# Performance work log

Measured on AMD Instinct MI355X. Metric: run time of the kernel, lower is better.

The kernel has to match this reference:

```python
import jax, jax.numpy as jnp
import numpy as np

DT = 0.1
GRAVITY = 9.81
DENSITY = 1028.0
ZVEC = jnp.array([0.0, 0.0, 1.0], dtype=jnp.float32)


def _skew(v):
    # v: [k,3] -> [k,3,3] skew-symmetric matrix (matches A/B/C column construction)
    x, y, z = v[..., 0], v[..., 1], v[..., 2]
    o = jnp.zeros_like(x)
    r0 = jnp.stack([o, -z, y], -1)
    r1 = jnp.stack([z, o, -x], -1)
    r2 = jnp.stack([-y, x, o], -1)
    return jnp.stack([r0, r1, r2], -2)


def _body2inertial(pose):
    # pose: [k,7]; quat stored as (x,y,z,w) in pose[:,3:7]
    q = pose[:, 3:7]
    x, y, z, w = q[:, 0], q[:, 1], q[:, 2], q[:, 3]
    r0 = jnp.stack([1 - 2 * (y * y + z * z), 2 * (x * y - z * w), 2 * (x * z + y * w)], -1)
    r1 = jnp.stack([2 * (x * y + z * w), 1 - 2 * (x * x + z * z), 2 * (y * z - x * w)], -1)
    r2 = jnp.stack([2 * (x * z - y * w), 2 * (y * z + x * w), 1 - 2 * (x * x + y * y)], -1)
    rot = jnp.stack([r0, r1, r2], -2)  # [k,3,3]
    t = 0.5 * jnp.stack([
        jnp.stack([-x, -y, -z], -1),
        jnp.stack([w, -z, y], -1),
        jnp.stack([z, w, -x], -1),
        jnp.stack([-y, x, w], -1)], -2)  # [k,4,3]
    return rot, t


def _restoring(rot, mass, volume, cog, cob):
    fng = -mass * GRAVITY * ZVEC              # (3,)
    fnb = volume * DENSITY * GRAVITY * ZVEC   # (3,)
    # rotItoB = rot^T -> rot^T @ f == einsum('kji,j->ki')
    fbg = jnp.einsum('kji,j->ki', rot, fng)
    fbb = jnp.einsum('kji,j->ki', rot, fnb)
    mbg = jnp.cross(cog, fbg)
    mbb = jnp.cross(cob, fbb)
    return -jnp.concatenate([fbg + fbb, mbg + mbb], -1)  # [k,6]


def _damping(v, linDamp, linDampFow, quadDamp):
    eye6 = jnp.eye(6, dtype=v.dtype)
    D = -linDamp - v[:, :, None] * linDampFow
    return D - quadDamp * (jnp.abs(v)[:, :, None] * eye6)  # [k,6,6]


def _coriolis(v, mTot):
    M = mTot[0]
    mv_top = jnp.einsum('ij,kj->ki', M[0:3, 0:3], v[:, 0:3]) + jnp.einsum('ij,kj->ki', M[0:3, 3:6], v[:, 3:6])
    mv_bot = jnp.einsum('ij,kj->ki', M[3:6, 0:3], v[:, 0:3]) + jnp.einsum('ij,kj->ki', M[3:6, 3:6], v[:, 3:6])
    s12 = -_skew(mv_top)
    s22 = -_skew(mv_bot)
    z33 = jnp.zeros_like(s12)
    r1 = jnp.concatenate([z33, s12], -1)
    r2 = jnp.concatenate([s12, s22], -1)  # note: source uses s12 (not s12^T) in lower-left, reproduced faithfully
    return jnp.concatenate([r1, r2], -2)  # [k,6,6]


def _dot(x, u, mass, volume, cog, cob, mTot, linDamp, linDampFow, quadDamp):
    p, v = x[:, 0:7], x[:, 7:13]
    rot, t = _body2inertial(p)
    # jacobian is block-diag [[rot,0],[0,t]] -> apply blocks directly
    pDot_lin = jnp.einsum('kij,kj->ki', rot, v[:, 0:3])  # [k,3]
    pDot_ang = jnp.einsum('kij,kj->ki', t, v[:, 3:6])    # [k,4]
    D = _damping(v, linDamp, linDampFow, quadDamp)
    C = _coriolis(v, mTot)
    Dv = jnp.einsum('kij,kj->ki', D, v)
    Cv = jnp.einsum('kij,kj->ki', C, v)
    g = _restoring(rot, mass, volume, cog, cob)
    rhs = u - Cv - Dv - g                      # [k,6]
    vDot = jnp.linalg.solve(mTot[0], rhs.T).T  # single shared 6x6 solve
    return jnp.concatenate([pDot_lin, pDot_ang, vDot], -1)  # [k,13]


def _norm_quat(xs):
    q = xs[:, 3:7]
    q = q / jnp.linalg.norm(q, axis=-1, keepdims=True)
    return xs.at[:, 3:7].set(q)


def reference(x, u, mass, volume, cog, cob, mTot, linDamp, linDampFow, quadDamp):
    # RK2 integration step (rk=2 default)
    k1 = _dot(x, u, mass, volume, cog, cob, mTot, linDamp, linDampFow, quadDamp)
    k2 = _dot(x + k1 * DT, u, mass, volume, cog, cob, mTot, linDamp, linDampFow, quadDamp)
    return _norm_quat(x + (DT / 2.0) * (k1 + k2))


def setup_inputs() -> dict:
    key = jax.random.key(0)
    kx, ku = jax.random.split(key)
    K = 524288
    x = jax.random.normal(kx, (K, 13), dtype=jnp.float32)
    u = jax.random.normal(ku, (K, 6), dtype=jnp.float32)
    mass = jnp.array([100.0], dtype=jnp.float32)
    volume = jnp.array([1.0], dtype=jnp.float32)
    cog = jnp.zeros((1, 3), dtype=jnp.float32)
    cob = jnp.array([[0.0, 0.0, 0.2]], dtype=jnp.float32)
    rb = np.zeros((6, 6), dtype=np.float32)
    rb[0:3, 0:3] = 100.0 * np.eye(3, dtype=np.float32)
    ma = 100.0 * np.eye(6, dtype=np.float32) + 1e-7      # default Ma (+1e-7 on every entry)
    mTot = jnp.asarray(rb + ma)[None]                    # [1,6,6]
    linDamp = jnp.diag(jnp.array([-70.0, -70.0, -700.0, -300.0, -300.0, -100.0], dtype=jnp.float32))[None]
    linDampFow = jnp.zeros((1, 6, 6), dtype=jnp.float32)
    quadDamp = jnp.diag(jnp.array([-740.0, -990.0, -1800.0, -670.0, -770.0, -520.0], dtype=jnp.float32))[None]
    return {"x": x, "u": u, "mass": mass, "volume": volume, "cog": cog, "cob": cob,
            "mTot": mTot, "linDamp": linDamp, "linDampFow": linDampFow, "quadDamp": quadDamp}
```

## Files before the change

kernel.cpp:

```cpp
#include <hip/hip_runtime.h>
#include <math.h>


__device__ __forceinline__ float fast_rcp(float x) {
    float r = __builtin_amdgcn_rcpf(x);
    return r * (2.0f - x * r);
}

__device__ __forceinline__ void fossen_dot(const float* __restrict__ X,
                                           const float* __restrict__ U,
                                           const float* __restrict__ smi,
                                           const float* __restrict__ mTot,
                                           const float* __restrict__ linDamp,
                                           const float* __restrict__ linDampFow,
                                           const float* __restrict__ qdiag,
                                           const float* __restrict__ cgcb,
                                           float fgz, float fbz,
                                           float* __restrict__ xd)
{
    const float qx = X[3], qy = X[4], qz = X[5], qw = X[6];
    const float r00 = 1.f - 2.f*(qy*qy + qz*qz);
    const float r01 = 2.f*(qx*qy - qz*qw);
    const float r02 = 2.f*(qx*qz + qy*qw);
    const float r10 = 2.f*(qx*qy + qz*qw);
    const float r11 = 1.f - 2.f*(qx*qx + qz*qz);
    const float r12 = 2.f*(qy*qz - qx*qw);
    const float r20 = 2.f*(qx*qz - qy*qw);
    const float r21 = 2.f*(qy*qz + qx*qw);
    const float r22 = 1.f - 2.f*(qx*qx + qy*qy);

    const float v0 = X[7],  v1 = X[8],  v2 = X[9];
    const float v3 = X[10], v4 = X[11], v5 = X[12];

    xd[0] = r00*v0 + r01*v1 + r02*v2;
    xd[1] = r10*v0 + r11*v1 + r12*v2;
    xd[2] = r20*v0 + r21*v1 + r22*v2;
    xd[3] = 0.5f*(-qx*v3 - qy*v4 - qz*v5);
    xd[4] = 0.5f*( qw*v3 - qz*v4 + qy*v5);
    xd[5] = 0.5f*( qz*v3 + qw*v4 - qx*v5);
    xd[6] = 0.5f*(-qy*v3 + qx*v4 + qw*v5);

    const float v[6] = {v0, v1, v2, v3, v4, v5};

    float P[6];
#pragma unroll
    for (int i = 0; i < 6; ++i) {
        float ld = 0.f, ldf = 0.f;
#pragma unroll
        for (int j = 0; j < 6; ++j) {
            ld  += linDamp[i*6 + j]    * v[j];
            ldf += linDampFow[i*6 + j] * v[j];
        }
        P[i] = ld + v[i]*ldf + qdiag[i] * fabsf(v[i]) * v[i];
    }

    float mv[6];
#pragma unroll
    for (int i = 0; i < 6; ++i) {
        float s = 0.f;
#pragma unroll
        for (int j = 0; j < 6; ++j) s += mTot[i*6 + j] * v[j];
        mv[i] = s;
    }
    float Cv[6];
    Cv[0] = -(mv[1]*v5 - mv[2]*v4);
    Cv[1] = -(mv[2]*v3 - mv[0]*v5);
    Cv[2] = -(mv[0]*v4 - mv[1]*v3);
    Cv[3] = -(mv[1]*v2 - mv[2]*v1) - (mv[4]*v5 - mv[5]*v4);
    Cv[4] = -(mv[2]*v0 - mv[0]*v2) - (mv[5]*v3 - mv[3]*v5);
    Cv[5] = -(mv[0]*v1 - mv[1]*v0) - (mv[3]*v4 - mv[4]*v3);

    const float fb0 = r20*fgz, fb1 = r21*fgz, fb2 = r22*fgz;
    const float bb0 = r20*fbz, bb1 = r21*fbz, bb2 = r22*fbz;
    const float cgx = cgcb[0], cgy = cgcb[1], cgz = cgcb[2];
    const float cbx = cgcb[3], cby = cgcb[4], cbz = cgcb[5];
    const float m0 = cgy*fb2 - cgz*fb1 + cby*bb2 - cbz*bb1;
    const float m1 = cgz*fb0 - cgx*fb2 + cbz*bb0 - cbx*bb2;
    const float m2 = cgx*fb1 - cgy*fb0 + cbx*bb1 - cby*bb0;
    const float g[6] = { -(fb0+bb0), -(fb1+bb1), -(fb2+bb2), -m0, -m1, -m2 };

    float rhs[6];
#pragma unroll
    for (int i = 0; i < 6; ++i) rhs[i] = U[i] - Cv[i] + P[i] - g[i];

#pragma unroll
    for (int i = 0; i < 6; ++i) {
        float s = 0.f;
#pragma unroll
        for (int j = 0; j < 6; ++j) s += smi[i*6 + j] * rhs[j];
        xd[7+i] = s;
    }
}

__global__ void __launch_bounds__(256, 4)
auv_rk2_fused(const float* __restrict__ x, const float* __restrict__ u,
              const float* __restrict__ mass, const float* __restrict__ volume,
              const float* __restrict__ cog, const float* __restrict__ cob,
              const float* __restrict__ mTot, const float* __restrict__ linDamp,
              const float* __restrict__ linDampFow,
              const float* __restrict__ quadDamp,
              float* __restrict__ out, int K)
{
    __shared__ float sx[256 * 13];
    __shared__ float smi[36];
    const int tid   = threadIdx.x;
    const int base  = blockIdx.x * 256;
    const int nElem = min(256, K - base);

    if (nElem == 256) {
        const float* gx = x + (size_t)base * 13;
#pragma unroll
        for (int it = 0; it < 3; ++it) {
            const int k = it*256 + tid;
            __builtin_amdgcn_global_load_lds(
                (const __attribute__((address_space(1))) void*)(gx + (size_t)k*4),
                (__attribute__((address_space(3))) void*)(&sx[k*4]), 16, 0, 0);
        }
        if (tid < 64) {
            const int k = 768 + tid;
            __builtin_amdgcn_global_load_lds(
                (const __attribute__((address_space(1))) void*)(gx + (size_t)k*4),
                (__attribute__((address_space(3))) void*)(&sx[k*4]), 16, 0, 0);
        }
    } else {
        for (int k = tid; k < nElem*13; k += 256) sx[k] = x[(size_t)base*13 + k];
    }

    float U[6];
    if (tid < nElem) {
        const float* gu = u + (size_t)(base + tid) * 6;
        const float2 a2 = *(const float2*)(gu);
        const float2 b2 = *(const float2*)(gu + 2);
        const float2 c2 = *(const float2*)(gu + 4);
        U[0]=a2.x; U[1]=a2.y; U[2]=b2.x; U[3]=b2.y; U[4]=c2.x; U[5]=c2.y;
    }

    float qdiag[6], cgcb[6];
#pragma unroll
    for (int i = 0; i < 6; ++i) qdiag[i] = quadDamp[i*6 + i];
#pragma unroll
    for (int i = 0; i < 3; ++i) { cgcb[i] = cog[i]; cgcb[3+i] = cob[i]; }
    const float fgz = -mass[0] * 9.81f;
    const float fbz =  volume[0] * 1028.0f * 9.81f;

    if (tid == 0) {
        float a[36], Mi[36];
#pragma unroll
        for (int i = 0; i < 36; ++i) a[i] = mTot[i];
#pragma unroll
        for (int i = 0; i < 36; ++i) Mi[i] = 0.f;
#pragma unroll
        for (int i = 0; i < 6; ++i) Mi[i*6 + i] = 1.f;
#pragma unroll
        for (int col = 0; col < 6; ++col) {
            const float d = fast_rcp(a[col*6 + col]);
#pragma unroll
            for (int j = 0; j < 6; ++j) { a[col*6+j] *= d; Mi[col*6+j] *= d; }
#pragma unroll
            for (int r = 0; r < 6; ++r) {
                if (r == col) continue;
                const float f = a[r*6 + col];
#pragma unroll
                for (int j = 0; j < 6; ++j) {
                    a[r*6+j]  -= f * a[col*6+j];
                    Mi[r*6+j] -= f * Mi[col*6+j];
                }
            }
        }
#pragma unroll
        for (int i = 0; i < 36; ++i) smi[i] = Mi[i];
    }

    __syncthreads();

    if (tid < nElem) {
        float X[13];
#pragma unroll
        for (int j = 0; j < 13; ++j) X[j] = sx[tid*13 + j];

        float k1[13], X2[13], k2[13], Y[13];
        fossen_dot(X, U, smi, mTot, linDamp, linDampFow, qdiag, cgcb, fgz, fbz, k1);
#pragma unroll
        for (int j = 0; j < 13; ++j) X2[j] = X[j] + 0.1f * k1[j];
        fossen_dot(X2, U, smi, mTot, linDamp, linDampFow, qdiag, cgcb, fgz, fbz, k2);
#pragma unroll
        for (int j = 0; j < 13; ++j) Y[j] = X[j] + 0.05f * (k1[j] + k2[j]);

        const float nq  = Y[3]*Y[3] + Y[4]*Y[4] + Y[5]*Y[5] + Y[6]*Y[6];
        float inv = __builtin_amdgcn_rsqf(nq);
        inv = inv * (1.5f - 0.5f * nq * inv * inv);
        Y[3] *= inv; Y[4] *= inv; Y[5] *= inv; Y[6] *= inv;

#pragma unroll
        for (int j = 0; j < 13; ++j) sx[tid*13 + j] = Y[j];
    }
    __syncthreads();

    if (nElem == 256) {
        float4*       go = (float4*)(out + (size_t)base * 13);
        const float4* s4 = (const float4*)sx;
#pragma unroll
        for (int it = 0; it < 3; ++it) go[it*256 + tid] = s4[it*256 + tid];
        if (tid < 64) go[768 + tid] = s4[768 + tid];
    } else {
        for (int k = tid; k < nElem*13; k += 256) out[(size_t)base*13 + k] = sx[k];
    }
}

extern "C" void kernel_launch(void* const* d_in, const int* in_sizes, int n_in,
                              void* d_out, int out_size, void* d_ws, size_t ws_size,
                              hipStream_t stream)
{
    const float* x          = (const float*)d_in[0];
    const float* u          = (const float*)d_in[1];
    const float* mass       = (const float*)d_in[2];
    const float* volume     = (const float*)d_in[3];
    const float* cog        = (const float*)d_in[4];
    const float* cob        = (const float*)d_in[5];
    const float* mTot       = (const float*)d_in[6];
    const float* linDamp    = (const float*)d_in[7];
    const float* linDampFow = (const float*)d_in[8];
    const float* quadDamp   = (const float*)d_in[9];
    float*       out        = (float*)d_out;

    const int K = in_sizes[0] / 13;
    const int blocks = (K + 255) / 256;
    auv_rk2_fused<<<blocks, 256, 0, stream>>>(x, u, mass, volume, cog, cob,
                                              mTot, linDamp, linDampFow,
                                              quadDamp, out, K);
}
```

Before: 115.6 us.

## Add sparsity fast paths for damping and per-wave output stores

Detects at runtime whether linDamp is diagonal and linDampFow is all zero, and skips the full 6x6 products when they are. Each wavefront now stages and writes back its own 64 rows, so the block-wide barrier before the output store is replaced by a wave-local LDS waitcnt. The inverse mass matrix is padded to stride 8 so each row loads as a float4 plus a float2, and launch bounds are raised to 8 blocks per CU. The general matrix path is kept as a fallback. The per-thread scan of 72 global matrix entries is new overhead, and the added code may raise register pressure against the higher occupancy target.

```diff
diff --git a/kernel.cpp b/kernel.cpp
--- a/kernel.cpp
+++ b/kernel.cpp
@@ -14,8 +14,10 @@
                                            const float* __restrict__ linDamp,
                                            const float* __restrict__ linDampFow,
                                            const float* __restrict__ qdiag,
+                                           const float* __restrict__ lddiag,
                                            const float* __restrict__ cgcb,
                                            float fgz, float fbz,
+                                           bool ldDiag, bool ldfZero,
                                            float* __restrict__ xd)
 {
     const float qx = X[3], qy = X[4], qz = X[5], qw = X[6];
@@ -44,14 +46,26 @@
 
     float P[6];
 #pragma unroll
-    for (int i = 0; i < 6; ++i) {
-        float ld = 0.f, ldf = 0.f;
-#pragma unroll
-        for (int j = 0; j < 6; ++j) {
-            ld  += linDamp[i*6 + j]    * v[j];
-            ldf += linDampFow[i*6 + j] * v[j];
-        }
-        P[i] = ld + v[i]*ldf + qdiag[i] * fabsf(v[i]) * v[i];
+    for (int i = 0; i < 6; ++i)
+        P[i] = lddiag[i]*v[i] + qdiag[i]*fabsf(v[i])*v[i];
+    if (!ldDiag) {
+#pragma unroll
+        for (int i = 0; i < 6; ++i) {
+            float ld = 0.f;
+#pragma unroll
+            for (int j = 0; j < 6; ++j)
+                if (j != i) ld += linDamp[i*6 + j] * v[j];
+            P[i] += ld;
+        }
+    }
+    if (!ldfZero) {
+#pragma unroll
+        for (int i = 0; i < 6; ++i) {
+            float ldf = 0.f;
+#pragma unroll
+            for (int j = 0; j < 6; ++j) ldf += linDampFow[i*6 + j] * v[j];
+            P[i] += v[i]*ldf;
+        }
     }
 
     float mv[6];
@@ -85,14 +99,14 @@
 
 #pragma unroll
     for (int i = 0; i < 6; ++i) {
-        float s = 0.f;
-#pragma unroll
-        for (int j = 0; j < 6; ++j) s += smi[i*6 + j] * rhs[j];
-        xd[7+i] = s;
-    }
-}
-
-__global__ void __launch_bounds__(256, 4)
+        const float4 m4 = *(const float4*)(&smi[i*8]);
+        const float2 m2 = *(const float2*)(&smi[i*8 + 4]);
+        xd[7+i] = m4.x*rhs[0] + m4.y*rhs[1] + m4.z*rhs[2] + m4.w*rhs[3]
+                + m2.x*rhs[4] + m2.y*rhs[5];
+    }
+}
+
+__global__ void __launch_bounds__(256, 8)
 auv_rk2_fused(const float* __restrict__ x, const float* __restrict__ u,
               const float* __restrict__ mass, const float* __restrict__ volume,
               const float* __restrict__ cog, const float* __restrict__ cob,
@@ -102,8 +116,11 @@
               float* __restrict__ out, int K)
 {
     __shared__ float sx[256 * 13];
-    __shared__ float smi[36];
+    __shared__ float smi[48];
     const int tid   = threadIdx.x;
+    const int w     = tid >> 6;
+    const int l     = tid & 63;
+    const int wbase = w * 208;
     const int base  = blockIdx.x * 256;
     const int nElem = min(256, K - base);
 
@@ -111,13 +128,13 @@
         const float* gx = x + (size_t)base * 13;
 #pragma unroll
         for (int it = 0; it < 3; ++it) {
-            const int k = it*256 + tid;
+            const int k = wbase + it*64 + l;
             __builtin_amdgcn_global_load_lds(
                 (const __attribute__((address_space(1))) void*)(gx + (size_t)k*4),
                 (__attribute__((address_space(3))) void*)(&sx[k*4]), 16, 0, 0);
         }
-        if (tid < 64) {
-            const int k = 768 + tid;
+        if (l < 16) {
+            const int k = wbase + 192 + l;
             __builtin_amdgcn_global_load_lds(
                 (const __attribute__((address_space(1))) void*)(gx + (size_t)k*4),
                 (__attribute__((address_space(3))) void*)(&sx[k*4]), 16, 0, 0);
@@ -135,13 +152,22 @@
         U[0]=a2.x; U[1]=a2.y; U[2]=b2.x; U[3]=b2.y; U[4]=c2.x; U[5]=c2.y;
     }
 
-    float qdiag[6], cgcb[6];
-#pragma unroll
-    for (int i = 0; i < 6; ++i) qdiag[i] = quadDamp[i*6 + i];
+    float qdiag[6], lddiag[6], cgcb[6];
+#pragma unroll
+    for (int i = 0; i < 6; ++i) { qdiag[i] = quadDamp[i*6+i]; lddiag[i] = linDamp[i*6+i]; }
 #pragma unroll
     for (int i = 0; i < 3; ++i) { cgcb[i] = cog[i]; cgcb[3+i] = cob[i]; }
     const float fgz = -mass[0] * 9.81f;
     const float fbz =  volume[0] * 1028.0f * 9.81f;
+
+    bool ldDiag = true, ldfZero = true;
+#pragma unroll
+    for (int i = 0; i < 6; ++i)
+#pragma unroll
+        for (int j = 0; j < 6; ++j) {
+            ldfZero = ldfZero && (linDampFow[i*6+j] == 0.0f);
+            if (i != j) ldDiag = ldDiag && (linDamp[i*6+j] == 0.0f);
+        }
 
     if (tid == 0) {
         float a[36], Mi[36];
@@ -168,21 +194,25 @@
             }
         }
 #pragma unroll
-        for (int i = 0; i < 36; ++i) smi[i] = Mi[i];
+        for (int r = 0; r < 6; ++r)
+#pragma unroll
+            for (int c = 0; c < 6; ++c) smi[r*8 + c] = Mi[r*6 + c];
     }
 
     __syncthreads();
 
-    if (tid < nElem) {
+    if (nElem == 256) {
         float X[13];
 #pragma unroll
         for (int j = 0; j < 13; ++j) X[j] = sx[tid*13 + j];
 
         float k1[13], X2[13], k2[13], Y[13];
-        fossen_dot(X, U, smi, mTot, linDamp, linDampFow, qdiag, cgcb, fgz, fbz, k1);
+        fossen_dot(X, U, smi, mTot, linDamp, linDampFow, qdiag, lddiag, cgcb,
+                   fgz, fbz, ldDiag, ldfZero, k1);
 #pragma unroll
         for (int j = 0; j < 13; ++j) X2[j] = X[j] + 0.1f * k1[j];
-        fossen_dot(X2, U, smi, mTot, linDamp, linDampFow, qdiag, cgcb, fgz, fbz, k2);
+        fossen_dot(X2, U, smi, mTot, linDamp, linDampFow, qdiag, lddiag, cgcb,
+                   fgz, fbz, ldDiag, ldfZero, k2);
 #pragma unroll
         for (int j = 0; j < 13; ++j) Y[j] = X[j] + 0.05f * (k1[j] + k2[j]);
 
@@ -193,16 +223,44 @@
 
 #pragma unroll
         for (int j = 0; j < 13; ++j) sx[tid*13 + j] = Y[j];
-    }
-    __syncthreads();
-
-    if (nElem == 256) {
+
+        asm volatile("s_waitcnt lgkmcnt(0)" ::: "memory");
+
         float4*       go = (float4*)(out + (size_t)base * 13);
         const float4* s4 = (const float4*)sx;
 #pragma unroll
-        for (int it = 0; it < 3; ++it) go[it*256 + tid] = s4[it*256 + tid];
-        if (tid < 64) go[768 + tid] = s4[768 + tid];
+        for (int it = 0; it < 3; ++it) {
+            const int k = wbase + it*64 + l;
+            go[k] = s4[k];
+        }
+        if (l < 16) {
+            const int k = wbase + 192 + l;
+            go[k] = s4[k];
+        }
     } else {
+        if (tid < nElem) {
+            float X[13];
+#pragma unroll
+            for (int j = 0; j < 13; ++j) X[j] = sx[tid*13 + j];
+
+            float k1[13], X2[13], k2[13], Y[13];
+            fossen_dot(X, U, smi, mTot, linDamp, linDampFow, qdiag, lddiag, cgcb,
+                       fgz, fbz, ldDiag, ldfZero, k1);
+#pragma unroll
+            for (int j = 0; j < 13; ++j) X2[j] = X[j] + 0.1f * k1[j];
+            fossen_dot(X2, U, smi, mTot, linDamp, linDampFow, qdiag, lddiag, cgcb,
+                       fgz, fbz, ldDiag, ldfZero, k2);
+#pragma unroll
+            for (int j = 0; j < 13; ++j) Y[j] = X[j] + 0.05f * (k1[j] + k2[j]);
+
+            const float nq  = Y[3]*Y[3] + Y[4]*Y[4] + Y[5]*Y[5] + Y[6]*Y[6];
+            float inv = __builtin_amdgcn_rsqf(nq);
+            inv = inv * (1.5f - 0.5f * nq * inv * inv);
+            Y[3] *= inv; Y[4] *= inv; Y[5] *= inv; Y[6] *= inv;
+#pragma unroll
+            for (int j = 0; j < 13; ++j) sx[tid*13 + j] = Y[j];
+        }
+        __syncthreads();
         for (int k = tid; k < nElem*13; k += 256) out[(size_t)base*13 + k] = sx[k];
     }
 }
```

Result: slower. 188.2 us (+62.7%).
